# Kernel optimization log

Hardware: AMD Instinct MI355X
Metric: run time of the kernel (lower is better)

The kernel has to match this reference:

```python
import jax, jax.numpy as jnp
import numpy as np

ALPHA = 0.2  # LeakyReLU negative slope
NEG_INF = -9e15


def setup_inputs() -> dict:
    key = jax.random.key(0)
    k1, k2, k3, k4 = jax.random.split(key, 4)
    B, N, F_IN, F_OUT = 2, 4096, 128, 64
    h = jax.random.normal(k1, (B, N, F_IN), dtype=jnp.float32)
    adj = jax.random.randint(k2, (N, N), 0, 2, dtype=jnp.int32)
    W = jax.random.normal(k3, (F_IN, F_OUT), dtype=jnp.float32) * (1.414 / np.sqrt(F_IN))
    a = jax.random.normal(k4, (2 * F_OUT, 1), dtype=jnp.float32) * 0.1
    return {"h": h, "adj": adj, "W": W, "a": a}


def reference(h, adj, W, a):
    # h: (B, N, F_in), adj: (N, N), W: (F_in, F_out), a: (2*F_out, 1)
    Wh = jnp.einsum("bnf,fo->bno", h, W)  # (B, N, F_out)
    F_out = W.shape[1]
    a1 = a[:F_out, 0]   # attends to source node i
    a2 = a[F_out:, 0]   # attends to target node j
    # e_ij = leakyrelu(a1.Wh_i + a2.Wh_j)  -- rank-1 decomposition of the
    # original cat([Wh_i, Wh_j]) @ a, identical math without O(N^2*2F) tensor.
    s1 = Wh @ a1  # (B, N)
    s2 = Wh @ a2  # (B, N)
    e = s1[:, :, None] + s2[:, None, :]  # (B, N, N)
    e = jnp.where(e >= 0, e, ALPHA * e)  # LeakyReLU
    scores = jnp.where(adj[None, :, :] > 0, e, NEG_INF)
    attention = jax.nn.softmax(scores, axis=-1)
    # dropout=0 (eval/deterministic baseline)
    h_prime = jnp.einsum("bij,bjo->bio", attention, Wh)  # (B, N, F_out)
    return jax.nn.elu(h_prime)  # concat=True branch
```

## Files before the change

kernel.cpp:

```cpp
#include <hip/hip_runtime.h>
#include <hip/hip_bf16.h>
#include <math.h>

#define NB 2
#define NN 4096
#define FIN 128
#define FOUT 64
#define LALPHA 0.2f

#define WS_S1    0
#define WS_S2    (NB*NN)
#define WS_WHT   (2*NB*NN)
#define WS_ABITS (WS_WHT + NB*FOUT*NN/2)


typedef __attribute__((ext_vector_type(8))) short short8;
typedef __attribute__((ext_vector_type(4))) float f32x4;

static __device__ inline unsigned int pack2bf(float x, float y) {
    float2 f2; f2.x = x; f2.y = y;
    __hip_bfloat162 pp = __float22bfloat162_rn(f2);
    return *reinterpret_cast<unsigned int*>(&pp);
}

#define GLL16(gsrc, ldst)                                                        \
    __builtin_amdgcn_global_load_lds(                                            \
        (const __attribute__((address_space(1))) void*)(gsrc),                   \
        (__attribute__((address_space(3))) void*)(ldst), 16, 0, 0)

__global__ __launch_bounds__(256) void k1_proj(const float* __restrict__ h,
                                               const float* __restrict__ W,
                                               const float* __restrict__ a,
                                               const int* __restrict__ adj,
                                               float* __restrict__ ws) {
    __shared__ float tbuf[4][68];
    int gid  = blockIdx.x * 256 + threadIdx.x;
    int wid  = gid >> 6;
    int lane = threadIdx.x & 63;
    int w    = threadIdx.x >> 6;

    int prow  = 2 * blockIdx.x + (threadIdx.x >> 7);
    int pword = threadIdx.x & 127;
    const int4* psrc = (const int4*)&adj[(size_t)prow * NN + pword * 32];
    int4 pv[8];
#pragma unroll
    for (int k = 0; k < 8; ++k) pv[k] = psrc[k];

    const float* hrow = h + (size_t)wid * FIN;
    float h0 = hrow[lane];
    float h1 = hrow[64 + lane];
    float acc = 0.f;
#pragma unroll
    for (int f = 0; f < 64; ++f) {
        float hf = __shfl(h0, f);
        acc = fmaf(hf, W[f * FOUT + lane], acc);
    }
#pragma unroll
    for (int f = 0; f < 64; ++f) {
        float hf = __shfl(h1, f);
        acc = fmaf(hf, W[(64 + f) * FOUT + lane], acc);
    }
    tbuf[w][lane] = acc;
    float v1 = acc * a[lane];
    float v2 = acc * a[FOUT + lane];
#pragma unroll
    for (int off = 32; off; off >>= 1) {
        v1 += __shfl_xor(v1, off);
        v2 += __shfl_xor(v2, off);
    }
    if (lane == 0) {
        ws[WS_S1 + wid] = v1 * 1.44269504088896f;
        ws[WS_S2 + wid] = v2 * 1.44269504088896f;
    }

    unsigned int bits = 0;
#pragma unroll
    for (int k = 0; k < 8; ++k) {
        bits |= (pv[k].x != 0 ? 1u : 0u) << (4 * k);
        bits |= (pv[k].y != 0 ? 1u : 0u) << (4 * k + 1);
        bits |= (pv[k].z != 0 ? 1u : 0u) << (4 * k + 2);
        bits |= (pv[k].w != 0 ? 1u : 0u) << (4 * k + 3);
    }
    ((unsigned int*)(ws + WS_ABITS))[(size_t)prow * 128 + pword] = bits;

    __syncthreads();
    if (threadIdx.x < 64) {
        int f = threadIdx.x;
        int wid0 = blockIdx.x * 4;
        int b  = wid0 >> 12;
        int n0 = wid0 & (NN - 1);
        unsigned short* whT = (unsigned short*)(ws + WS_WHT);
        uint2 pk;
        pk.x = pack2bf(tbuf[0][f], tbuf[1][f]);
        pk.y = pack2bf(tbuf[2][f], tbuf[3][f]);
        size_t off = ((size_t)(b * 128 + (n0 >> 5)) * 2048) + f * 32 + (n0 & 31);
        *(uint2*)&whT[off] = pk;
    }
}

__global__ __launch_bounds__(1024, 4) void k3_attn(const float* __restrict__ ws,
                                                   float* __restrict__ out) {
    __shared__ float redbuf[16 * 2048];
    __shared__ float s2buf[16][256];
    __shared__ float lred[16][32];
    const int tid  = threadIdx.x;
    const int w    = tid >> 6;
    const int lane = tid & 63;
    const int col  = lane & 15;
    const int quad = lane >> 4;
    const int rt   = blockIdx.x & 127;
    const int b    = blockIdx.x >> 7;
    const int i0   = rt * 32;
    const int jbase = w * 256;

    const float* __restrict__ s1 = ws + WS_S1 + b * NN;
    const float* __restrict__ s2 = ws + WS_S2 + b * NN;
    const unsigned short* __restrict__ whT =
        (const unsigned short*)(ws + WS_WHT) + (size_t)b * FOUT * NN;
    const unsigned int* __restrict__ abits = (const unsigned int*)(ws + WS_ABITS);

    char* slot = (char*)redbuf + w * 8192;
    float* s2s = s2buf[w];
    const unsigned short* wsrc = whT + (size_t)w * 8 * 2048;
    const int lsrc = col * 32 + quad * 8;

    unsigned int mrow[2][8];
#pragma unroll
    for (int g = 0; g < 2; ++g) {
        const int4* mp = (const int4*)&abits[(size_t)(i0 + g * 16 + col) * 128 + w * 8];
        *(int4*)&mrow[g][0] = mp[0];
        *(int4*)&mrow[g][4] = mp[1];
    }
    float s1a[2];
#pragma unroll
    for (int g = 0; g < 2; ++g) s1a[g] = s1[i0 + g * 16 + col];
    asm volatile("s_waitcnt vmcnt(0)" ::: "memory");

#define ISSUE_TILE(ks, sl)                                                \
    do {                                                                  \
        const unsigned short* wb_ = wsrc + (size_t)(ks) * 2048;           \
        GLL16(wb_ + 0 * 512 + lsrc, slot + (sl) * 4096 + 0 * 1024);       \
        GLL16(wb_ + 1 * 512 + lsrc, slot + (sl) * 4096 + 1 * 1024);       \
        GLL16(wb_ + 2 * 512 + lsrc, slot + (sl) * 4096 + 2 * 1024);       \
        GLL16(wb_ + 3 * 512 + lsrc, slot + (sl) * 4096 + 3 * 1024);       \
    } while (0)

    GLL16(&s2[jbase] + lane * 4, s2s);
    ISSUE_TILE(0, 0);
    ISSUE_TILE(1, 1);
    asm volatile("s_waitcnt vmcnt(8)" ::: "memory");

    f32x4 acc[2][4];
    float lsum[2] = {0.f, 0.f};
#pragma unroll
    for (int g = 0; g < 2; ++g)
#pragma unroll
        for (int nt = 0; nt < 4; ++nt) acc[g][nt] = (f32x4)0.f;

#pragma unroll
    for (int ks = 0; ks < 8; ++ks) {
        const int sl = ks & 1;

        float4 s2lo = *(const float4*)&s2s[ks * 32 + quad * 8];
        float4 s2hi = *(const float4*)&s2s[ks * 32 + quad * 8 + 4];
        float sj[8] = {s2lo.x, s2lo.y, s2lo.z, s2lo.w,
                       s2hi.x, s2hi.y, s2hi.z, s2hi.w};
        short8 afrag[2];
#pragma unroll
        for (int g = 0; g < 2; ++g) {
            const unsigned int mb = (mrow[g][ks] >> (quad * 8)) & 0xffu;
            float p[8];
#pragma unroll
            for (int jj = 0; jj < 8; ++jj) {
                float e = s1a[g] + sj[jj];
                e = fmaxf(e, LALPHA * e);
                float pe = exp2f(e);
                p[jj] = ((mb >> jj) & 1u) ? pe : 0.f;
                lsum[g] += p[jj];
            }
            unsigned int pk[4];
#pragma unroll
            for (int q = 0; q < 4; ++q) pk[q] = pack2bf(p[2 * q], p[2 * q + 1]);
            afrag[g] = *(short8*)pk;
        }

        __builtin_amdgcn_sched_barrier(0);
        if (ks == 7) asm volatile("s_waitcnt vmcnt(0)" ::: "memory");
        else         asm volatile("s_waitcnt vmcnt(4)" ::: "memory");

        __builtin_amdgcn_s_setprio(1);
#pragma unroll
        for (int nt = 0; nt < 4; ++nt) {
            short8 bf = *(const short8*)(slot + sl * 4096 + nt * 1024 + lane * 16);
            acc[0][nt] = __builtin_amdgcn_mfma_f32_16x16x32_bf16(
                afrag[0], bf, acc[0][nt], 0, 0, 0);
            acc[1][nt] = __builtin_amdgcn_mfma_f32_16x16x32_bf16(
                afrag[1], bf, acc[1][nt], 0, 0, 0);
        }
        __builtin_amdgcn_s_setprio(0);
        if (ks < 6) ISSUE_TILE(ks + 2, sl);
    }

    float* red_w = redbuf + w * 2048;
#pragma unroll
    for (int g = 0; g < 2; ++g) {
        float v = lsum[g];
        v += __shfl_xor(v, 16);
        v += __shfl_xor(v, 32);
        if (quad == 0) lred[w][g * 16 + col] = v;
#pragma unroll
        for (int nt = 0; nt < 4; ++nt)
#pragma unroll
            for (int reg = 0; reg < 4; ++reg)
                red_w[g * 1024 + ((nt * 4 + reg) << 6) + lane] = acc[g][nt][reg];
    }
    __syncthreads();

#pragma unroll
    for (int e = 0; e < 2; ++e) {
        int flat = e * 1024 + tid;
        int f    = flat & 63;
        int r32  = flat >> 6;
        int g    = r32 >> 4;
        int r16  = r32 & 15;
        int q2   = r16 >> 2, reg = r16 & 3;
        int c2   = f & 15,   nt  = f >> 4;
        int ln   = q2 * 16 + c2;
        int off  = g * 1024 + ((nt * 4 + reg) << 6) + ln;
        float acv = 0.f, l = 0.f;
#pragma unroll
        for (int ww = 0; ww < 16; ++ww) {
            acv += redbuf[ww * 2048 + off];
            l   += lred[ww][g * 16 + r16];
        }
        float v = acv / l;
        out[((size_t)(b * NN + i0 + r32) << 6) + f] = v > 0.f ? v : (__expf(v) - 1.f);
    }
}

extern "C" void kernel_launch(void* const* d_in, const int* in_sizes, int n_in,
                              void* d_out, int out_size, void* d_ws, size_t ws_size,
                              hipStream_t stream) {
    const float* h   = (const float*)d_in[0];
    const int*   adj = (const int*)d_in[1];
    const float* W   = (const float*)d_in[2];
    const float* a   = (const float*)d_in[3];
    float* ws  = (float*)d_ws;
    float* out = (float*)d_out;

    hipLaunchKernelGGL(k1_proj, dim3(NB * NN / 4), dim3(256), 0, stream, h, W, a, adj, ws);
    hipLaunchKernelGGL(k3_attn, dim3(256), dim3(1024), 0, stream, ws, out);
}
```

Before: 140.3 us.

## Coalesce adjacency loads, stage h in LDS, interleave batch blocks in attention

In the projection kernel, each lane now reads adjacency int4s at a 64-element stride, so a wavefront's loads are contiguous instead of each thread reading 32 consecutive ints. Per-lane nibbles are combined into 32-bit mask words with xor shuffles. The h row is staged in LDS and read as float4 broadcasts instead of one shuffle per feature. The attention kernel maps the low block-index bit to the batch, so both batches' blocks for the same row tile run at the same time and can share adjacency-mask reads in cache. The cost is extra shuffles and partial-lane stores for the mask packing.

```diff
diff --git a/kernel.cpp b/kernel.cpp
--- a/kernel.cpp
+++ b/kernel.cpp
@@ -33,32 +33,31 @@
                                                const float* __restrict__ a,
                                                const int* __restrict__ adj,
                                                float* __restrict__ ws) {
+    __shared__ __align__(16) float hbuf[4][128];
     __shared__ float tbuf[4][68];
     int gid  = blockIdx.x * 256 + threadIdx.x;
     int wid  = gid >> 6;
     int lane = threadIdx.x & 63;
     int w    = threadIdx.x >> 6;
 
-    int prow  = 2 * blockIdx.x + (threadIdx.x >> 7);
-    int pword = threadIdx.x & 127;
-    const int4* psrc = (const int4*)&adj[(size_t)prow * NN + pword * 32];
+    int prow = 2 * blockIdx.x + (w >> 1);
+    const int4* psrc = (const int4*)(adj + (size_t)prow * NN + (w & 1) * 2048);
     int4 pv[8];
 #pragma unroll
-    for (int k = 0; k < 8; ++k) pv[k] = psrc[k];
+    for (int k = 0; k < 8; ++k) pv[k] = psrc[k * 64 + lane];
 
     const float* hrow = h + (size_t)wid * FIN;
-    float h0 = hrow[lane];
-    float h1 = hrow[64 + lane];
+    hbuf[w][lane]      = hrow[lane];
+    hbuf[w][64 + lane] = hrow[64 + lane];
+
     float acc = 0.f;
 #pragma unroll
-    for (int f = 0; f < 64; ++f) {
-        float hf = __shfl(h0, f);
-        acc = fmaf(hf, W[f * FOUT + lane], acc);
-    }
-#pragma unroll
-    for (int f = 0; f < 64; ++f) {
-        float hf = __shfl(h1, f);
-        acc = fmaf(hf, W[(64 + f) * FOUT + lane], acc);
+    for (int f4 = 0; f4 < 32; ++f4) {
+        float4 hv = *(const float4*)&hbuf[w][f4 * 4];
+        acc = fmaf(hv.x, W[(f4 * 4 + 0) * FOUT + lane], acc);
+        acc = fmaf(hv.y, W[(f4 * 4 + 1) * FOUT + lane], acc);
+        acc = fmaf(hv.z, W[(f4 * 4 + 2) * FOUT + lane], acc);
+        acc = fmaf(hv.w, W[(f4 * 4 + 3) * FOUT + lane], acc);
     }
     tbuf[w][lane] = acc;
     float v1 = acc * a[lane];
@@ -73,15 +72,20 @@
         ws[WS_S2 + wid] = v2 * 1.44269504088896f;
     }
 
-    unsigned int bits = 0;
+    unsigned int* ab = (unsigned int*)(ws + WS_ABITS);
 #pragma unroll
     for (int k = 0; k < 8; ++k) {
-        bits |= (pv[k].x != 0 ? 1u : 0u) << (4 * k);
-        bits |= (pv[k].y != 0 ? 1u : 0u) << (4 * k + 1);
-        bits |= (pv[k].z != 0 ? 1u : 0u) << (4 * k + 2);
-        bits |= (pv[k].w != 0 ? 1u : 0u) << (4 * k + 3);
-    }
-    ((unsigned int*)(ws + WS_ABITS))[(size_t)prow * 128 + pword] = bits;
+        unsigned int nib = (pv[k].x != 0 ? 1u : 0u)
+                         | (pv[k].y != 0 ? 2u : 0u)
+                         | (pv[k].z != 0 ? 4u : 0u)
+                         | (pv[k].w != 0 ? 8u : 0u);
+        unsigned int val = nib << ((lane & 7) * 4);
+        val |= __shfl_xor(val, 1);
+        val |= __shfl_xor(val, 2);
+        val |= __shfl_xor(val, 4);
+        if ((lane & 7) == 0)
+            ab[(size_t)prow * 128 + (w & 1) * 64 + k * 8 + (lane >> 3)] = val;
+    }
 
     __syncthreads();
     if (threadIdx.x < 64) {
@@ -108,8 +112,8 @@
     const int lane = tid & 63;
     const int col  = lane & 15;
     const int quad = lane >> 4;
-    const int rt   = blockIdx.x & 127;
-    const int b    = blockIdx.x >> 7;
+    const int rt   = blockIdx.x >> 1;
+    const int b    = blockIdx.x & 1;
     const int i0   = rt * 32;
     const int jbase = w * 256;
 
```

Result: faster. 135.7 us (-3.3%).
